# Kernel optimization log

Hardware: AMD Instinct MI355X
Metric: run time of the kernel (lower is better)

## Reference

```python
import jax, jax.numpy as jnp
import numpy as np

E, H, HD = 2048, 32, 64
SCALE = HD ** -0.5


def setup_inputs() -> dict:
    key = jax.random.key(0)
    ks = jax.random.split(key, 11)
    B, T, P = 16, 4, 4096
    S = P + T
    return {
        "hidden_states": jax.random.normal(ks[0], (B, T, E), jnp.float32),
        "past_key": jax.random.normal(ks[1], (1, H, P, HD), jnp.float32),
        "past_value": jax.random.normal(ks[2], (1, H, P, HD), jnp.float32),
        "attention_mask": jnp.zeros((B, 1, T, S), jnp.float32),
        "Wq": jax.random.normal(ks[3], (E, E), jnp.float32) * 0.02,
        "bq": jax.random.normal(ks[4], (E,), jnp.float32) * 0.02,
        "Wk": jax.random.normal(ks[5], (E, E), jnp.float32) * 0.02,
        "bk": jax.random.normal(ks[6], (E,), jnp.float32) * 0.02,
        "Wv": jax.random.normal(ks[7], (E, E), jnp.float32) * 0.02,
        "bv": jax.random.normal(ks[8], (E,), jnp.float32) * 0.02,
        "Wo": jax.random.normal(ks[9], (E, E), jnp.float32) * 0.02,
        "bo": jax.random.normal(ks[10], (E,), jnp.float32) * 0.02,
    }


def _shape(x, B, S):
    # [B,S,E] -> [B,H,S,hd]
    return x.reshape(B, S, H, HD).transpose(0, 2, 1, 3)


def reference(hidden_states, past_key, past_value, attention_mask,
              Wq, bq, Wk, bk, Wv, bv, Wo, bo):
    B, T, _ = hidden_states.shape
    # projections (torch Linear: x @ W.T + b); query pre-scaled
    q = _shape(hidden_states @ Wq.T + bq, B, T) * SCALE   # [B,H,T,hd]
    k_new = _shape(hidden_states @ Wk.T + bk, B, T)       # [B,H,T,hd]
    v_new = _shape(hidden_states @ Wv.T + bv, B, T)
    # cache stored with batch 1, broadcast (torch repeat) to B, then concat
    k_past = jnp.broadcast_to(past_key, (B,) + past_key.shape[1:])
    v_past = jnp.broadcast_to(past_value, (B,) + past_value.shape[1:])
    k = jnp.concatenate([k_past, k_new], axis=2)          # [B,H,S,hd]
    v = jnp.concatenate([v_past, v_new], axis=2)
    scores = jnp.einsum('bhtd,bhsd->bhts', q, k)          # [B,H,T,S]
    scores = scores + attention_mask                      # mask is [B,1,T,S]
    scores = jnp.maximum(scores, jnp.finfo(scores.dtype).min)
    w = jax.nn.softmax(scores, axis=-1)
    out = jnp.einsum('bhts,bhsd->bhtd', w, v)             # [B,H,T,hd]
    out = out.transpose(0, 2, 1, 3).reshape(B, T, E)
    return out @ Wo.T + bo
```

## Files before the change

kernel.cpp:

```cpp
#include <hip/hip_runtime.h>
#include <hip/hip_bf16.h>


typedef float f4 __attribute__((ext_vector_type(4)));
typedef short s8v __attribute__((ext_vector_type(8)));

#define NEG_HUGE (-3.402823466e38f)

__device__ inline unsigned short f2bs(float x) {
  union { float f; unsigned int u; } a; a.f = x;
  unsigned int u = a.u;
  u += 0x7fffu + ((u >> 16) & 1u);
  return (unsigned short)(u >> 16);
}
__device__ inline float bs2f(unsigned short s) {
  union { unsigned int u; float f; } a; a.u = ((unsigned int)s) << 16;
  return a.f;
}
__device__ inline unsigned int pk2(float a, float b) {
  union { __hip_bfloat162 v; unsigned int u; } c;
  c.v = __float22bfloat162_rn(make_float2(a, b));
  return c.u;
}
__device__ inline unsigned long long pack4(float a, float b, float c, float d) {
  return (unsigned long long)pk2(a, b) | ((unsigned long long)pk2(c, d) << 32);
}
__device__ inline s8v cvt8(f4 a, f4 b) {
  union { s8v s; unsigned int u[4]; } r;
  r.u[0] = pk2(a[0], a[1]); r.u[1] = pk2(a[2], a[3]);
  r.u[2] = pk2(b[0], b[1]); r.u[3] = pk2(b[2], b[3]);
  return r.s;
}
__device__ inline f4 mfma16(s8v a, s8v b, f4 c) {
  return __builtin_amdgcn_mfma_f32_16x16x32_bf16(a, b, c, 0, 0, 0);
}
__device__ inline f4 fzero() { f4 z = {0.f,0.f,0.f,0.f}; return z; }
__device__ inline float wave_sum(float v) {
  #pragma unroll
  for (int off = 32; off; off >>= 1) v += __shfl_xor(v, off, 64);
  return v;
}

__global__ __launch_bounds__(256) void k_qkv(
    const float* __restrict__ hs, const float* __restrict__ Wq,
    const float* __restrict__ Wk, const float* __restrict__ Wv,
    float* __restrict__ part) {
  __shared__ __align__(16) unsigned short As[64 * 264];
  const int n0 = blockIdx.x * 64;
  const int ksb = blockIdx.y;
  const int p = n0 >> 11;
  const int c0 = n0 & 2047;
  const float* W = (p == 0) ? Wq : (p == 1) ? Wk : Wv;
  const int t = threadIdx.x, lane = t & 63, w = t >> 6;
  const int cl = lane & 15, quad = lane >> 4;

  f4 acc[4];
  #pragma unroll
  for (int i = 0; i < 4; ++i) acc[i] = fzero();

  const int cw = c0 + w * 16 + cl;
  for (int kt = 0; kt < 2; ++kt) {
    const int k0 = ksb * 512 + kt * 256;
    __syncthreads();
    #pragma unroll
    for (int i = 0; i < 16; ++i) {
      int idx4 = t + (i << 8);
      int row = idx4 >> 6;
      int col = (idx4 & 63) << 2;
      f4 v = *reinterpret_cast<const f4*>(hs + row * 2048 + k0 + col);
      *reinterpret_cast<unsigned long long*>(&As[row * 264 + col]) =
          pack4(v[0], v[1], v[2], v[3]);
    }
    __syncthreads();
    const float* wbase = W + (size_t)cw * 2048 + k0;
    #pragma unroll
    for (int ks2 = 0; ks2 < 8; ++ks2) {
      const int kb = ks2 * 32 + quad * 8;
      f4 w0 = *reinterpret_cast<const f4*>(wbase + kb);
      f4 w1 = *reinterpret_cast<const f4*>(wbase + kb + 4);
      s8v bf = cvt8(w0, w1);
      #pragma unroll
      for (int mt = 0; mt < 4; ++mt) {
        s8v af = *reinterpret_cast<const s8v*>(&As[(mt * 16 + cl) * 264 + kb]);
        acc[mt] = mfma16(af, bf, acc[mt]);
      }
    }
  }
  float* outp = part + (size_t)ksb * 64 * 6144;
  #pragma unroll
  for (int mt = 0; mt < 4; ++mt)
    #pragma unroll
    for (int rg = 0; rg < 4; ++rg) {
      int r = mt * 16 + quad * 4 + rg;
      outp[r * 6144 + n0 + w * 16 + cl] = acc[mt][rg];
    }
}

__global__ __launch_bounds__(256) void k_qkv_red(
    const float* __restrict__ part, const float* __restrict__ bq,
    const float* __restrict__ bk, const float* __restrict__ bv,
    unsigned short* __restrict__ qws, float* __restrict__ knew,
    float* __restrict__ vnew) {
  int idx = blockIdx.x * 256 + threadIdx.x;
  int r = idx / 6144;
  int n = idx - r * 6144;
  float s = part[idx] + part[idx + 393216] + part[idx + 786432] + part[idx + 1179648];
  int c = n & 2047, p = n >> 11;
  int h = c >> 6, d = c & 63;
  int b = r >> 2, tt = r & 3;
  if (p == 0) {
    s = (s + bq[c]) * 0.125f;
    qws[h * 4608 + r * 72 + d] = f2bs(s);
  } else if (p == 1) {
    knew[((h * 16 + b) * 4 + tt) * 64 + d] = s + bk[c];
  } else {
    vnew[((h * 16 + b) * 4 + tt) * 64 + d] = s + bv[c];
  }
}

__global__ __launch_bounds__(256) void k_flash(
    const unsigned short* __restrict__ qws, const float* __restrict__ Kp,
    const float* __restrict__ Vp, const float* __restrict__ mask,
    float* __restrict__ Opart, float* __restrict__ mpart,
    float* __restrict__ lpart) {
  __shared__ __align__(16) unsigned short Pl[64 * 264];
  __shared__ float redm[4 * 64];
  __shared__ float reds[4 * 64];
  const int bx = blockIdx.x;
  const int h = bx & 31, cch = bx >> 5;
  const int s0 = cch * 256;
  const int t = threadIdx.x, lane = t & 63, w = t >> 6;
  const int cl = lane & 15, quad = lane >> 4;
  const float* Kh = Kp + (size_t)h * 4096 * 64;
  const float* Vh = Vp + (size_t)h * 4096 * 64;

  s8v qf[4][2];
  #pragma unroll
  for (int qt = 0; qt < 4; ++qt)
    #pragma unroll
    for (int k2 = 0; k2 < 2; ++k2)
      qf[qt][k2] = *reinterpret_cast<const s8v*>(
          qws + h * 4608 + (qt * 16 + cl) * 72 + k2 * 32 + quad * 8);

  f4 acc[4][4];
  #pragma unroll
  for (int si = 0; si < 4; ++si)
    #pragma unroll
    for (int qt = 0; qt < 4; ++qt) acc[si][qt] = fzero();

  #pragma unroll
  for (int si = 0; si < 4; ++si) {
    const float* kr = Kh + (size_t)(s0 + w * 64 + si * 16 + cl) * 64 + quad * 8;
    #pragma unroll
    for (int k2 = 0; k2 < 2; ++k2) {
      f4 k0v = *reinterpret_cast<const f4*>(kr + k2 * 32);
      f4 k1v = *reinterpret_cast<const f4*>(kr + k2 * 32 + 4);
      s8v ak = cvt8(k0v, k1v);
      #pragma unroll
      for (int qt = 0; qt < 4; ++qt)
        acc[si][qt] = mfma16(ak, qf[qt][k2], acc[si][qt]);
    }
  }

  #pragma unroll
  for (int si = 0; si < 4; ++si)
    #pragma unroll
    for (int qt = 0; qt < 4; ++qt) {
      f4 mv = *reinterpret_cast<const f4*>(
          mask + (size_t)(qt * 16 + cl) * 4100 + s0 + w * 64 + si * 16 + quad * 4);
      #pragma unroll
      for (int rg = 0; rg < 4; ++rg)
        acc[si][qt][rg] = fmaxf(acc[si][qt][rg] + mv[rg], NEG_HUGE);
    }

  #pragma unroll
  for (int qt = 0; qt < 4; ++qt) {
    float m = NEG_HUGE;
    #pragma unroll
    for (int si = 0; si < 4; ++si)
      #pragma unroll
      for (int rg = 0; rg < 4; ++rg) m = fmaxf(m, acc[si][qt][rg]);
    m = fmaxf(m, __shfl_xor(m, 16, 64));
    m = fmaxf(m, __shfl_xor(m, 32, 64));
    if (quad == 0) redm[w * 64 + qt * 16 + cl] = m;
  }
  __syncthreads();

  float mq[4];
  #pragma unroll
  for (int qt = 0; qt < 4; ++qt) {
    int q = qt * 16 + cl;
    mq[qt] = fmaxf(fmaxf(redm[q], redm[64 + q]),
                   fmaxf(redm[128 + q], redm[192 + q]));
    if (w == 0 && quad == 0) mpart[(h * 16 + cch) * 64 + q] = mq[qt];
  }
  #pragma unroll
  for (int qt = 0; qt < 4; ++qt) {
    float sum = 0.f;
    #pragma unroll
    for (int si = 0; si < 4; ++si) {
      f4 e;
      #pragma unroll
      for (int rg = 0; rg < 4; ++rg) {
        e[rg] = __expf(acc[si][qt][rg] - mq[qt]);
        sum += e[rg];
      }
      uint2 pw;
      pw.x = pk2(e[0], e[1]);
      pw.y = pk2(e[2], e[3]);
      *reinterpret_cast<uint2*>(
          &Pl[(qt * 16 + cl) * 264 + w * 64 + si * 16 + quad * 4]) = pw;
    }
    sum += __shfl_xor(sum, 16, 64);
    sum += __shfl_xor(sum, 32, 64);
    if (quad == 0) reds[w * 64 + qt * 16 + cl] = sum;
  }
  __syncthreads();

  if (w == 0 && quad == 0) {
    #pragma unroll
    for (int qt = 0; qt < 4; ++qt) {
      int q = qt * 16 + cl;
      lpart[(h * 16 + cch) * 64 + q] =
          reds[q] + reds[64 + q] + reds[128 + q] + reds[192 + q];
    }
  }

  f4 oacc[4];
  #pragma unroll
  for (int mt = 0; mt < 4; ++mt) oacc[mt] = fzero();
  const int dcol = w * 16 + cl;
  #pragma unroll
  for (int k2 = 0; k2 < 8; ++k2) {
    const int sb = k2 * 32 + quad * 8;
    const float* vb = Vh + (size_t)(s0 + sb) * 64 + dcol;
    f4 v0, v1;
    v0[0] = vb[0];   v0[1] = vb[64];  v0[2] = vb[128]; v0[3] = vb[192];
    v1[0] = vb[256]; v1[1] = vb[320]; v1[2] = vb[384]; v1[3] = vb[448];
    s8v bv = cvt8(v0, v1);
    #pragma unroll
    for (int mt = 0; mt < 4; ++mt) {
      s8v pa = *reinterpret_cast<const s8v*>(&Pl[(mt * 16 + cl) * 264 + sb]);
      oacc[mt] = mfma16(pa, bv, oacc[mt]);
    }
  }
  float* ob = Opart + (size_t)(h * 16 + cch) * 64 * 64;
  #pragma unroll
  for (int mt = 0; mt < 4; ++mt)
    #pragma unroll
    for (int rg = 0; rg < 4; ++rg)
      ob[(mt * 16 + quad * 4 + rg) * 64 + dcol] = oacc[mt][rg];
}

__global__ __launch_bounds__(64) void k_merge(
    const unsigned short* __restrict__ qws, const float* __restrict__ knew,
    const float* __restrict__ vnew, const float* __restrict__ mask,
    const float* __restrict__ Opart, const float* __restrict__ mpart,
    const float* __restrict__ lpart, unsigned short* __restrict__ attn) {
  const int bx = blockIdx.x;
  const int h = bx & 31, b = bx >> 5;
  const int d = threadIdx.x;
  for (int tt = 0; tt < 4; ++tt) {
    const int r = b * 4 + tt;
    float qd = bs2f(qws[h * 4608 + r * 72 + d]);
    float scn[4];
    #pragma unroll
    for (int tp = 0; tp < 4; ++tp) {
      float kn = knew[((h * 16 + b) * 4 + tp) * 64 + d];
      float s = wave_sum(qd * kn);
      s += mask[(size_t)r * 4100 + 4096 + tp];
      scn[tp] = fmaxf(s, NEG_HUGE);
    }
    float mi[16], li[16];
    float mtot = NEG_HUGE;
    #pragma unroll
    for (int i = 0; i < 16; ++i) {
      mi[i] = mpart[(h * 16 + i) * 64 + r];
      li[i] = lpart[(h * 16 + i) * 64 + r];
      mtot = fmaxf(mtot, mi[i]);
    }
    #pragma unroll
    for (int tp = 0; tp < 4; ++tp) mtot = fmaxf(mtot, scn[tp]);
    float ltot = 0.f, od = 0.f;
    #pragma unroll
    for (int i = 0; i < 16; ++i) {
      float fct = __expf(mi[i] - mtot);
      ltot += li[i] * fct;
      od += Opart[((size_t)(h * 16 + i) * 64 + r) * 64 + d] * fct;
    }
    #pragma unroll
    for (int tp = 0; tp < 4; ++tp) {
      float e = __expf(scn[tp] - mtot);
      ltot += e;
      od += e * vnew[((h * 16 + b) * 4 + tp) * 64 + d];
    }
    attn[(size_t)r * 2048 + h * 64 + d] = f2bs(od / ltot);
  }
}

__global__ __launch_bounds__(256) void k_out(
    const unsigned short* __restrict__ attn, const float* __restrict__ Wo,
    float* __restrict__ part) {
  __shared__ __align__(16) unsigned short As[64 * 264];
  const int n0 = blockIdx.x * 64;
  const int ksb = blockIdx.y;
  const int k0 = ksb * 256;
  const int t = threadIdx.x, lane = t & 63, w = t >> 6;
  const int cl = lane & 15, quad = lane >> 4;
  #pragma unroll
  for (int i = 0; i < 8; ++i) {
    int idx8 = t + (i << 8);
    int row = idx8 >> 5;
    int col = (idx8 & 31) << 3;
    *reinterpret_cast<uint4*>(&As[row * 264 + col]) =
        *reinterpret_cast<const uint4*>(attn + (size_t)row * 2048 + k0 + col);
  }
  __syncthreads();
  f4 acc[4];
  #pragma unroll
  for (int i = 0; i < 4; ++i) acc[i] = fzero();
  const int cw = n0 + w * 16 + cl;
  const float* wbase = Wo + (size_t)cw * 2048 + k0;
  #pragma unroll
  for (int ks2 = 0; ks2 < 8; ++ks2) {
    const int kb = ks2 * 32 + quad * 8;
    f4 w0 = *reinterpret_cast<const f4*>(wbase + kb);
    f4 w1 = *reinterpret_cast<const f4*>(wbase + kb + 4);
    s8v bf = cvt8(w0, w1);
    #pragma unroll
    for (int mt = 0; mt < 4; ++mt) {
      s8v af = *reinterpret_cast<const s8v*>(&As[(mt * 16 + cl) * 264 + kb]);
      acc[mt] = mfma16(af, bf, acc[mt]);
    }
  }
  float* op = part + (size_t)ksb * 64 * 2048;
  #pragma unroll
  for (int mt = 0; mt < 4; ++mt)
    #pragma unroll
    for (int rg = 0; rg < 4; ++rg) {
      int r = mt * 16 + quad * 4 + rg;
      op[r * 2048 + n0 + w * 16 + cl] = acc[mt][rg];
    }
}

__global__ __launch_bounds__(256) void k_out_red(
    const float* __restrict__ part, const float* __restrict__ bo,
    float* __restrict__ out) {
  int idx = blockIdx.x * 256 + threadIdx.x;
  int n = idx & 2047;
  float s = bo[n];
  #pragma unroll
  for (int ks = 0; ks < 8; ++ks) s += part[idx + ks * 131072];
  out[idx] = s;
}

extern "C" void kernel_launch(void* const* d_in, const int* in_sizes, int n_in,
                              void* d_out, int out_size, void* d_ws, size_t ws_size,
                              hipStream_t stream) {
  const float* hs   = (const float*)d_in[0];
  const float* pk   = (const float*)d_in[1];
  const float* pv   = (const float*)d_in[2];
  const float* mask = (const float*)d_in[3];
  const float* Wq   = (const float*)d_in[4];
  const float* bq   = (const float*)d_in[5];
  const float* Wk   = (const float*)d_in[6];
  const float* bk   = (const float*)d_in[7];
  const float* Wv   = (const float*)d_in[8];
  const float* bv   = (const float*)d_in[9];
  const float* Wo   = (const float*)d_in[10];
  const float* bo   = (const float*)d_in[11];

  float* f = (float*)d_ws;
  float* qkv_part = f;
  float* o_part   = qkv_part + 1572864;
  float* Opart    = o_part   + 1048576;
  float* mpart    = Opart    + 2097152;
  float* lpart    = mpart    + 32768;
  float* knew     = lpart    + 32768;
  float* vnew     = knew     + 131072;
  unsigned short* qws  = (unsigned short*)(vnew + 131072);
  unsigned short* attn = qws + 147456;

  k_qkv<<<dim3(96, 4), 256, 0, stream>>>(hs, Wq, Wk, Wv, qkv_part);
  k_qkv_red<<<1536, 256, 0, stream>>>(qkv_part, bq, bk, bv, qws, knew, vnew);
  k_flash<<<512, 256, 0, stream>>>(qws, pk, pv, mask, Opart, mpart, lpart);
  k_merge<<<512, 64, 0, stream>>>(qws, knew, vnew, mask, Opart, mpart, lpart, attn);
  k_out<<<dim3(32, 8), 256, 0, stream>>>(attn, Wo, o_part);
  k_out_red<<<512, 256, 0, stream>>>(o_part, bo, (float*)d_out);
}
```

Before: 210.3 us.

## Drop split-K in QKV GEMM, fuse bias epilogue, retile output GEMM

The QKV projection moves from a split-K GEMM plus a separate reduction kernel to one kernel. It uses 16-column tiles over the full K dimension, reads operands straight from global memory with no LDS staging, and applies bias, scaling and the head-layout scatter in the epilogue. The output projection is retiled to 16-column tiles with split-K of 2, and its reduction is vectorised. The merge kernel now runs the 4 query rows as 4 waves in parallel instead of a serial loop. Together this removes one launch and the large partial-sum round trip through memory. The cost is that each block rereads the shared activation rows from global memory instead of LDS, and each block has less parallel work along K.

```diff
diff --git a/kernel.cpp b/kernel.cpp
--- a/kernel.cpp
+++ b/kernel.cpp
@@ -22,9 +22,6 @@
   c.v = __float22bfloat162_rn(make_float2(a, b));
   return c.u;
 }
-__device__ inline unsigned long long pack4(float a, float b, float c, float d) {
-  return (unsigned long long)pk2(a, b) | ((unsigned long long)pk2(c, d) << 32);
-}
 __device__ inline s8v cvt8(f4 a, f4 b) {
   union { s8v s; unsigned int u[4]; } r;
   r.u[0] = pk2(a[0], a[1]); r.u[1] = pk2(a[2], a[3]);
@@ -41,80 +38,53 @@
   return v;
 }
 
-__global__ __launch_bounds__(256) void k_qkv(
+__global__ __launch_bounds__(256) void k_qkv_f(
     const float* __restrict__ hs, const float* __restrict__ Wq,
     const float* __restrict__ Wk, const float* __restrict__ Wv,
-    float* __restrict__ part) {
-  __shared__ __align__(16) unsigned short As[64 * 264];
-  const int n0 = blockIdx.x * 64;
-  const int ksb = blockIdx.y;
+    const float* __restrict__ bq, const float* __restrict__ bk,
+    const float* __restrict__ bv,
+    unsigned short* __restrict__ qws, float* __restrict__ knew,
+    float* __restrict__ vnew) {
+  const int n0 = blockIdx.x * 16;
   const int p = n0 >> 11;
   const int c0 = n0 & 2047;
   const float* W = (p == 0) ? Wq : (p == 1) ? Wk : Wv;
   const int t = threadIdx.x, lane = t & 63, w = t >> 6;
   const int cl = lane & 15, quad = lane >> 4;
 
-  f4 acc[4];
-  #pragma unroll
-  for (int i = 0; i < 4; ++i) acc[i] = fzero();
-
-  const int cw = c0 + w * 16 + cl;
-  for (int kt = 0; kt < 2; ++kt) {
-    const int k0 = ksb * 512 + kt * 256;
-    __syncthreads();
-    #pragma unroll
-    for (int i = 0; i < 16; ++i) {
-      int idx4 = t + (i << 8);
-      int row = idx4 >> 6;
-      int col = (idx4 & 63) << 2;
-      f4 v = *reinterpret_cast<const f4*>(hs + row * 2048 + k0 + col);
-      *reinterpret_cast<unsigned long long*>(&As[row * 264 + col]) =
-          pack4(v[0], v[1], v[2], v[3]);
-    }
-    __syncthreads();
-    const float* wbase = W + (size_t)cw * 2048 + k0;
-    #pragma unroll
-    for (int ks2 = 0; ks2 < 8; ++ks2) {
-      const int kb = ks2 * 32 + quad * 8;
-      f4 w0 = *reinterpret_cast<const f4*>(wbase + kb);
-      f4 w1 = *reinterpret_cast<const f4*>(wbase + kb + 4);
-      s8v bf = cvt8(w0, w1);
-      #pragma unroll
-      for (int mt = 0; mt < 4; ++mt) {
-        s8v af = *reinterpret_cast<const s8v*>(&As[(mt * 16 + cl) * 264 + kb]);
-        acc[mt] = mfma16(af, bf, acc[mt]);
-      }
-    }
-  }
-  float* outp = part + (size_t)ksb * 64 * 6144;
-  #pragma unroll
-  for (int mt = 0; mt < 4; ++mt)
-    #pragma unroll
-    for (int rg = 0; rg < 4; ++rg) {
-      int r = mt * 16 + quad * 4 + rg;
-      outp[r * 6144 + n0 + w * 16 + cl] = acc[mt][rg];
-    }
-}
-
-__global__ __launch_bounds__(256) void k_qkv_red(
-    const float* __restrict__ part, const float* __restrict__ bq,
-    const float* __restrict__ bk, const float* __restrict__ bv,
-    unsigned short* __restrict__ qws, float* __restrict__ knew,
-    float* __restrict__ vnew) {
-  int idx = blockIdx.x * 256 + threadIdx.x;
-  int r = idx / 6144;
-  int n = idx - r * 6144;
-  float s = part[idx] + part[idx + 393216] + part[idx + 786432] + part[idx + 1179648];
-  int c = n & 2047, p = n >> 11;
-  int h = c >> 6, d = c & 63;
-  int b = r >> 2, tt = r & 3;
-  if (p == 0) {
-    s = (s + bq[c]) * 0.125f;
-    qws[h * 4608 + r * 72 + d] = f2bs(s);
-  } else if (p == 1) {
-    knew[((h * 16 + b) * 4 + tt) * 64 + d] = s + bk[c];
-  } else {
-    vnew[((h * 16 + b) * 4 + tt) * 64 + d] = s + bv[c];
+  const float* arow = hs + (size_t)(w * 16 + cl) * 2048 + quad * 8;
+  const float* brow = W + (size_t)(c0 + cl) * 2048 + quad * 8;
+
+  f4 acc0 = fzero(), acc1 = fzero();
+  #pragma unroll 4
+  for (int ks = 0; ks < 64; ks += 2) {
+    f4 a0 = *reinterpret_cast<const f4*>(arow + ks * 32);
+    f4 a1 = *reinterpret_cast<const f4*>(arow + ks * 32 + 4);
+    f4 b0 = *reinterpret_cast<const f4*>(brow + ks * 32);
+    f4 b1 = *reinterpret_cast<const f4*>(brow + ks * 32 + 4);
+    acc0 = mfma16(cvt8(a0, a1), cvt8(b0, b1), acc0);
+    f4 a2 = *reinterpret_cast<const f4*>(arow + ks * 32 + 32);
+    f4 a3 = *reinterpret_cast<const f4*>(arow + ks * 32 + 36);
+    f4 b2 = *reinterpret_cast<const f4*>(brow + ks * 32 + 32);
+    f4 b3 = *reinterpret_cast<const f4*>(brow + ks * 32 + 36);
+    acc1 = mfma16(cvt8(a2, a3), cvt8(b2, b3), acc1);
+  }
+
+  const int n = c0 + cl;
+  const int h = n >> 6, d = n & 63;
+  const float bias = (p == 0) ? bq[n] : (p == 1) ? bk[n] : bv[n];
+  #pragma unroll
+  for (int rg = 0; rg < 4; ++rg) {
+    const int r = w * 16 + quad * 4 + rg;
+    const int b = r >> 2, tt = r & 3;
+    float s = acc0[rg] + acc1[rg] + bias;
+    if (p == 0) {
+      qws[h * 4608 + r * 72 + d] = f2bs(s * 0.125f);
+    } else if (p == 1) {
+      knew[((h * 16 + b) * 4 + tt) * 64 + d] = s;
+    } else {
+      vnew[((h * 16 + b) * 4 + tt) * 64 + d] = s;
+    }
   }
 }
 
@@ -237,11 +207,11 @@
     f4 v0, v1;
     v0[0] = vb[0];   v0[1] = vb[64];  v0[2] = vb[128]; v0[3] = vb[192];
     v1[0] = vb[256]; v1[1] = vb[320]; v1[2] = vb[384]; v1[3] = vb[448];
-    s8v bv = cvt8(v0, v1);
+    s8v bvv = cvt8(v0, v1);
     #pragma unroll
     for (int mt = 0; mt < 4; ++mt) {
       s8v pa = *reinterpret_cast<const s8v*>(&Pl[(mt * 16 + cl) * 264 + sb]);
-      oacc[mt] = mfma16(pa, bv, oacc[mt]);
+      oacc[mt] = mfma16(pa, bvv, oacc[mt]);
     }
   }
   float* ob = Opart + (size_t)(h * 16 + cch) * 64 * 64;
@@ -252,106 +222,91 @@
       ob[(mt * 16 + quad * 4 + rg) * 64 + dcol] = oacc[mt][rg];
 }
 
-__global__ __launch_bounds__(64) void k_merge(
+__global__ __launch_bounds__(256) void k_merge(
     const unsigned short* __restrict__ qws, const float* __restrict__ knew,
     const float* __restrict__ vnew, const float* __restrict__ mask,
     const float* __restrict__ Opart, const float* __restrict__ mpart,
     const float* __restrict__ lpart, unsigned short* __restrict__ attn) {
   const int bx = blockIdx.x;
   const int h = bx & 31, b = bx >> 5;
-  const int d = threadIdx.x;
-  for (int tt = 0; tt < 4; ++tt) {
-    const int r = b * 4 + tt;
-    float qd = bs2f(qws[h * 4608 + r * 72 + d]);
-    float scn[4];
-    #pragma unroll
-    for (int tp = 0; tp < 4; ++tp) {
-      float kn = knew[((h * 16 + b) * 4 + tp) * 64 + d];
-      float s = wave_sum(qd * kn);
-      s += mask[(size_t)r * 4100 + 4096 + tp];
-      scn[tp] = fmaxf(s, NEG_HUGE);
-    }
-    float mi[16], li[16];
-    float mtot = NEG_HUGE;
-    #pragma unroll
-    for (int i = 0; i < 16; ++i) {
-      mi[i] = mpart[(h * 16 + i) * 64 + r];
-      li[i] = lpart[(h * 16 + i) * 64 + r];
-      mtot = fmaxf(mtot, mi[i]);
-    }
-    #pragma unroll
-    for (int tp = 0; tp < 4; ++tp) mtot = fmaxf(mtot, scn[tp]);
-    float ltot = 0.f, od = 0.f;
-    #pragma unroll
-    for (int i = 0; i < 16; ++i) {
-      float fct = __expf(mi[i] - mtot);
-      ltot += li[i] * fct;
-      od += Opart[((size_t)(h * 16 + i) * 64 + r) * 64 + d] * fct;
-    }
-    #pragma unroll
-    for (int tp = 0; tp < 4; ++tp) {
-      float e = __expf(scn[tp] - mtot);
-      ltot += e;
-      od += e * vnew[((h * 16 + b) * 4 + tp) * 64 + d];
-    }
-    attn[(size_t)r * 2048 + h * 64 + d] = f2bs(od / ltot);
-  }
+  const int tt = threadIdx.x >> 6;
+  const int d = threadIdx.x & 63;
+  const int r = b * 4 + tt;
+  float qd = bs2f(qws[h * 4608 + r * 72 + d]);
+  float scn[4];
+  #pragma unroll
+  for (int tp = 0; tp < 4; ++tp) {
+    float kn = knew[((h * 16 + b) * 4 + tp) * 64 + d];
+    float s = wave_sum(qd * kn);
+    s += mask[(size_t)r * 4100 + 4096 + tp];
+    scn[tp] = fmaxf(s, NEG_HUGE);
+  }
+  float mi[16], li[16];
+  float mtot = NEG_HUGE;
+  #pragma unroll
+  for (int i = 0; i < 16; ++i) {
+    mi[i] = mpart[(h * 16 + i) * 64 + r];
+    li[i] = lpart[(h * 16 + i) * 64 + r];
+    mtot = fmaxf(mtot, mi[i]);
+  }
+  #pragma unroll
+  for (int tp = 0; tp < 4; ++tp) mtot = fmaxf(mtot, scn[tp]);
+  float ltot = 0.f, od = 0.f;
+  #pragma unroll
+  for (int i = 0; i < 16; ++i) {
+    float fct = __expf(mi[i] - mtot);
+    ltot += li[i] * fct;
+    od += Opart[((size_t)(h * 16 + i) * 64 + r) * 64 + d] * fct;
+  }
+  #pragma unroll
+  for (int tp = 0; tp < 4; ++tp) {
+    float e = __expf(scn[tp] - mtot);
+    ltot += e;
+    od += e * vnew[((h * 16 + b) * 4 + tp) * 64 + d];
+  }
+  attn[(size_t)r * 2048 + h * 64 + d] = f2bs(od / ltot);
 }
 
 __global__ __launch_bounds__(256) void k_out(
     const unsigned short* __restrict__ attn, const float* __restrict__ Wo,
     float* __restrict__ part) {
-  __shared__ __align__(16) unsigned short As[64 * 264];
-  const int n0 = blockIdx.x * 64;
-  const int ksb = blockIdx.y;
-  const int k0 = ksb * 256;
+  const int n0 = blockIdx.x * 16;
+  const int k0 = blockIdx.y * 1024;
   const int t = threadIdx.x, lane = t & 63, w = t >> 6;
   const int cl = lane & 15, quad = lane >> 4;
-  #pragma unroll
-  for (int i = 0; i < 8; ++i) {
-    int idx8 = t + (i << 8);
-    int row = idx8 >> 5;
-    int col = (idx8 & 31) << 3;
-    *reinterpret_cast<uint4*>(&As[row * 264 + col]) =
-        *reinterpret_cast<const uint4*>(attn + (size_t)row * 2048 + k0 + col);
-  }
-  __syncthreads();
-  f4 acc[4];
-  #pragma unroll
-  for (int i = 0; i < 4; ++i) acc[i] = fzero();
-  const int cw = n0 + w * 16 + cl;
-  const float* wbase = Wo + (size_t)cw * 2048 + k0;
-  #pragma unroll
-  for (int ks2 = 0; ks2 < 8; ++ks2) {
-    const int kb = ks2 * 32 + quad * 8;
-    f4 w0 = *reinterpret_cast<const f4*>(wbase + kb);
-    f4 w1 = *reinterpret_cast<const f4*>(wbase + kb + 4);
-    s8v bf = cvt8(w0, w1);
-    #pragma unroll
-    for (int mt = 0; mt < 4; ++mt) {
-      s8v af = *reinterpret_cast<const s8v*>(&As[(mt * 16 + cl) * 264 + kb]);
-      acc[mt] = mfma16(af, bf, acc[mt]);
-    }
-  }
-  float* op = part + (size_t)ksb * 64 * 2048;
-  #pragma unroll
-  for (int mt = 0; mt < 4; ++mt)
-    #pragma unroll
-    for (int rg = 0; rg < 4; ++rg) {
-      int r = mt * 16 + quad * 4 + rg;
-      op[r * 2048 + n0 + w * 16 + cl] = acc[mt][rg];
-    }
+  const unsigned short* arow = attn + (size_t)(w * 16 + cl) * 2048 + k0 + quad * 8;
+  const float* brow = Wo + (size_t)(n0 + cl) * 2048 + k0 + quad * 8;
+  f4 acc0 = fzero(), acc1 = fzero();
+  #pragma unroll 4
+  for (int ks = 0; ks < 32; ks += 2) {
+    s8v a0 = *reinterpret_cast<const s8v*>(arow + ks * 32);
+    f4 b0 = *reinterpret_cast<const f4*>(brow + ks * 32);
+    f4 b1 = *reinterpret_cast<const f4*>(brow + ks * 32 + 4);
+    acc0 = mfma16(a0, cvt8(b0, b1), acc0);
+    s8v a1 = *reinterpret_cast<const s8v*>(arow + ks * 32 + 32);
+    f4 b2 = *reinterpret_cast<const f4*>(brow + ks * 32 + 32);
+    f4 b3 = *reinterpret_cast<const f4*>(brow + ks * 32 + 36);
+    acc1 = mfma16(a1, cvt8(b2, b3), acc1);
+  }
+  float* op = part + (size_t)blockIdx.y * 131072;
+  #pragma unroll
+  for (int rg = 0; rg < 4; ++rg) {
+    const int r = w * 16 + quad * 4 + rg;
+    op[r * 2048 + n0 + cl] = acc0[rg] + acc1[rg];
+  }
 }
 
 __global__ __launch_bounds__(256) void k_out_red(
     const float* __restrict__ part, const float* __restrict__ bo,
     float* __restrict__ out) {
-  int idx = blockIdx.x * 256 + threadIdx.x;
-  int n = idx & 2047;
-  float s = bo[n];
-  #pragma unroll
-  for (int ks = 0; ks < 8; ++ks) s += part[idx + ks * 131072];
-  out[idx] = s;
+  const int i4 = blockIdx.x * 256 + threadIdx.x;
+  f4 a = *reinterpret_cast<const f4*>(part + (size_t)i4 * 4);
+  f4 b = *reinterpret_cast<const f4*>(part + 131072 + (size_t)i4 * 4);
+  f4 bias = *reinterpret_cast<const f4*>(bo + (i4 & 511) * 4);
+  f4 o;
+  #pragma unroll
+  for (int rg = 0; rg < 4; ++rg) o[rg] = a[rg] + b[rg] + bias[rg];
+  *reinterpret_cast<f4*>(out + (size_t)i4 * 4) = o;
 }
 
 extern "C" void kernel_launch(void* const* d_in, const int* in_sizes, int n_in,
@@ -371,20 +326,18 @@
   const float* bo   = (const float*)d_in[11];
 
   float* f = (float*)d_ws;
-  float* qkv_part = f;
-  float* o_part   = qkv_part + 1572864;
-  float* Opart    = o_part   + 1048576;
-  float* mpart    = Opart    + 2097152;
-  float* lpart    = mpart    + 32768;
-  float* knew     = lpart    + 32768;
-  float* vnew     = knew     + 131072;
+  float* o_part = f;
+  float* Opart  = o_part + 262144;
+  float* mpart  = Opart  + 2097152;
+  float* lpart  = mpart  + 32768;
+  float* knew   = lpart  + 32768;
+  float* vnew   = knew   + 131072;
   unsigned short* qws  = (unsigned short*)(vnew + 131072);
   unsigned short* attn = qws + 147456;
 
-  k_qkv<<<dim3(96, 4), 256, 0, stream>>>(hs, Wq, Wk, Wv, qkv_part);
-  k_qkv_red<<<1536, 256, 0, stream>>>(qkv_part, bq, bk, bv, qws, knew, vnew);
+  k_qkv_f<<<384, 256, 0, stream>>>(hs, Wq, Wk, Wv, bq, bk, bv, qws, knew, vnew);
   k_flash<<<512, 256, 0, stream>>>(qws, pk, pv, mask, Opart, mpart, lpart);
-  k_merge<<<512, 64, 0, stream>>>(qws, knew, vnew, mask, Opart, mpart, lpart, attn);
-  k_out<<<dim3(32, 8), 256, 0, stream>>>(attn, Wo, o_part);
-  k_out_red<<<512, 256, 0, stream>>>(o_part, bo, (float*)d_out);
-}
+  k_merge<<<512, 256, 0, stream>>>(qws, knew, vnew, mask, Opart, mpart, lpart, attn);
+  k_out<<<dim3(128, 2), 256, 0, stream>>>(attn, Wo, o_part);
+  k_out_red<<<128, 256, 0, stream>>>(o_part, bo, (float*)d_out);
+}
```

Result: slower. 245.2 us (+16.6%).
